# Kernel tuning notes

Hardware: AMD Instinct MI355X
Metric: run time of the kernel (lower is better)

## Reference

```python
import jax, jax.numpy as jnp
import numpy as np

# --- model hyperparams (match init_kwargs) ---
N_DIM = 200      # n_dim == nfeat == nhidden (Linear(200,200) hardcoded in source)
NHID = 200
NLAYERS = 8
ALPHA = 0.1
LAMDA = 0.5
B, L = 20, 100   # dialogues x uniform dialogue length
N = B * L        # 2000 utterances per modality -> 3N = 6000 graph nodes
A_DIM, V_DIM, L_DIM, NSPK = 300, 342, 1024, 2


def _linear_params(key, fin, fout):
    s = 1.0 / np.sqrt(fin)
    k1, k2 = jax.random.split(key)
    W = jax.random.uniform(k1, (fin, fout), jnp.float32, -s, s)
    b = jax.random.uniform(k2, (fout,), jnp.float32, -s, s)
    return W, b


def setup_inputs() -> dict:
    key = jax.random.key(0)
    ks = jax.random.split(key, 12)
    a = jax.random.normal(ks[0], (N, A_DIM), jnp.float32)
    v = jax.random.normal(ks[1], (N, V_DIM), jnp.float32)
    l = jax.random.normal(ks[2], (N, L_DIM), jnp.float32)
    qmask = jax.random.uniform(ks[3], (L, B, NSPK), dtype=jnp.float32)
    # dense normalized adjacency over the 3N-node multimodal graph
    adj = jax.random.uniform(ks[4], (3 * N, 3 * N), dtype=jnp.float32) / (3.0 * N)
    Wa, ba = _linear_params(ks[5], A_DIM, N_DIM)
    Wv, bv = _linear_params(ks[6], V_DIM, N_DIM)
    Wl, bl = _linear_params(ks[7], L_DIM, N_DIM)
    spk_emb = jax.random.normal(ks[8], (NSPK, N_DIM), jnp.float32)
    W0, b0 = _linear_params(ks[9], N_DIM, NHID)
    s = 1.0 / np.sqrt(NHID)
    # variant=True -> conv weight is [2*nhidden, nhidden]
    convW = jax.random.uniform(ks[10], (NLAYERS, 2 * NHID, NHID), jnp.float32, -s, s)
    return dict(a=a, v=v, l=l, qmask=qmask, adj=adj,
                Wa=Wa, ba=ba, Wv=Wv, bv=bv, Wl=Wl, bl=bl,
                spk_emb=spk_emb, W0=W0, b0=b0, convW=convW, dia_len=L)


def reference(a, v, l, qmask, adj, Wa, ba, Wv, bv, Wl, bl, spk_emb, W0, b0, convW, dia_len):
    # modality projections
    a = a @ Wa + ba                                   # [N, n_dim]
    v = v @ Wv + bv
    l = l @ Wl + bl
    # qmask: [L, B, n_spk] seq-first -> concat per dialogue (uniform lengths)
    qcat = jnp.transpose(qmask[:dia_len], (1, 0, 2)).reshape(-1, qmask.shape[-1])  # [N, n_spk]
    spk_idx = jnp.argmax(qcat, axis=-1)
    l = l + spk_emb[spk_idx]                          # use_speaker, 'l' in modals
    # big multimodal graph: stack modalities along node axis
    x = jnp.concatenate([a, v, l], axis=0)            # [3N, n_dim]
    # GCNII_lyc (eval mode: dropout identity)
    h0 = jax.nn.relu(x @ W0 + b0)                     # [3N, nhidden]
    thetas = jnp.log(LAMDA / jnp.arange(1, NLAYERS + 1, dtype=jnp.float32) + 1.0)

    def layer(h, wt):
        W, theta = wt
        hi = adj @ h                                  # spmm (dense here)
        support = jnp.concatenate([hi, h0], axis=1)   # variant=True
        r = (1.0 - ALPHA) * hi + ALPHA * h0
        h_new = jax.nn.relu(theta * (support @ W) + (1.0 - theta) * r)
        return h_new, None

    h, _ = jax.lax.scan(layer, h0, (convW, thetas))
    feat = jnp.concatenate([x, h], axis=1)            # use_residue -> [3N, n_dim+nhidden]
    n = a.shape[0]
    # split modality chunks back and fuse on feature axis -> [N, 3*(n_dim+nhidden)]
    return jnp.concatenate([feat[:n], feat[n:2 * n], feat[2 * n:3 * n]], axis=-1)
```

## Files before the change

kernel.cpp:

```cpp
#include <hip/hip_runtime.h>
#include <math.h>

typedef unsigned short u16;
typedef unsigned int u32;
typedef __bf16 bf8_t __attribute__((ext_vector_type(8)));
typedef float f4_t __attribute__((ext_vector_type(4)));
typedef u16 us8_t __attribute__((ext_vector_type(8)));
typedef u16 us4_t __attribute__((ext_vector_type(4)));

#define LDC 224
#define NROWS 6016
#define PLANE (NROWS*LDC)

__device__ __forceinline__ float b2f(u16 x){
  union{u32 u; float f;} c; c.u = ((u32)x)<<16; return c.f;
}
__device__ __forceinline__ u16 f2b(float f){
  union{u32 u; float f;} c; c.f = f;
  u32 b = c.u;
  return (u16)((b + 0x7FFFu + ((b>>16)&1u)) >> 16);
}
__device__ __forceinline__ u16 ldcvt(const void* p, size_t i, int f){
  return f ? f2b(((const float*)p)[i]) : ((const u16*)p)[i];
}
__device__ __forceinline__ void gl16(const u16* g, u16* l){
  __builtin_amdgcn_global_load_lds((const __attribute__((address_space(1))) void*)g,
                                   (__attribute__((address_space(3))) void*)l, 16, 0, 0);
}

__global__ void detect_kernel(const u16* __restrict__ adj, int* __restrict__ flag)
{
  int l = threadIdx.x;
  u16 u = adj[2*l];
  int ex = (u >> 7) & 0xFF;
  bool ok = ((u >> 15) == 0) && (ex >= 0x30) && (ex <= 0x72);
  unsigned long long m = __ballot(ok);
  if (l == 0) flag[0] = (__popcll(m) < 32) ? 1 : 0;
}

__global__ void conv_kernel(const int* __restrict__ flag, const void* __restrict__ adj,
                            u16* __restrict__ adj_bf)
{
  const int f = flag[0];
  size_t idx = (size_t)blockIdx.x*256 + threadIdx.x;
  if (idx >= (size_t)6016*752) return;
  int row = (int)(idx / 752);
  int k8  = (int)(idx - (size_t)row*752) * 8;
  us8_t vv;
  if (row < 6000){
    if (f){
      const float* src = (const float*)adj + (size_t)row*6000;
      if (k8 + 8 <= 6000){
        f4_t x0 = *(const f4_t*)(src + k8);
        f4_t x1 = *(const f4_t*)(src + k8 + 4);
        #pragma unroll
        for (int j=0;j<4;j++){ vv[j] = f2b(x0[j]); vv[4+j] = f2b(x1[j]); }
      } else {
        #pragma unroll
        for (int j=0;j<8;j++){ int k=k8+j; vv[j] = (k<6000) ? f2b(src[k]) : (u16)0; }
      }
    } else {
      const u16* src = (const u16*)adj + (size_t)row*6000;
      if (k8 + 8 <= 6000){
        vv = *(const us8_t*)(src + k8);
      } else {
        #pragma unroll
        for (int j=0;j<8;j++){ int k=k8+j; vv[j] = (k<6000) ? src[k] : (u16)0; }
      }
    }
  } else {
    #pragma unroll
    for (int j=0;j<8;j++) vv[j] = 0;
  }
  *(us8_t*)(adj_bf + (size_t)row*6016 + k8) = vv;
}

__global__ void prep_kernel(const int* __restrict__ flag,
                            const void* __restrict__ Wa, const void* __restrict__ Wv,
                            const void* __restrict__ Wl, const void* __restrict__ W0,
                            const void* __restrict__ convW, const void* __restrict__ qmask,
                            const void* __restrict__ a_in, const void* __restrict__ v_in,
                            const void* __restrict__ l_in, const void* __restrict__ spkemb_in,
                            const void* __restrict__ ba, const void* __restrict__ bv,
                            const void* __restrict__ bl, const void* __restrict__ b0,
                            u16* __restrict__ WaT, u16* __restrict__ WvT, u16* __restrict__ WlT,
                            u16* __restrict__ W0T, u16* __restrict__ WtT, u16* __restrict__ WbT,
                            int* __restrict__ spk, u16* __restrict__ x_bf,
                            u16* __restrict__ a_p, u16* __restrict__ v_p, u16* __restrict__ l_p,
                            u16* __restrict__ spkem, u16* __restrict__ b_all)
{
  const int f = flag[0];
  const int y = blockIdx.y;
  const int e = blockIdx.x*256 + threadIdx.x;

  if (y < 20){
    const void* src; u16* dst; int K, kpad; size_t soff = 0;
    if (y == 0){ src=Wa; dst=WaT; K=300; kpad=320; }
    else if (y == 1){ src=Wv; dst=WvT; K=342; kpad=384; }
    else if (y == 2){ src=Wl; dst=WlT; K=1024; kpad=1024; }
    else if (y == 3){ src=W0; dst=W0T; K=200; kpad=256; }
    else if (y < 12){ int i=y-4;  src=convW; soff=(size_t)i*80000;          dst=WtT + i*57344; K=200; kpad=256; }
    else            { int i=y-12; src=convW; soff=(size_t)i*80000 + 40000;  dst=WbT + i*57344; K=200; kpad=256; }
    int total = 224*kpad;
    if (e >= total) return;
    int n = e / kpad, k = e - n*kpad;
    u16 val = 0;
    if (k < K && n < 200) val = ldcvt(src, soff + (size_t)k*200 + n, f);
    dst[e] = val;
    return;
  }
  if (y == 20){
    if (e < 2000){
      int b = e/100, t = e - b*100;
      size_t base = ((size_t)t*20 + b)*2;
      bool one;
      if (f) one = ((const float*)qmask)[base+1] > ((const float*)qmask)[base];
      else   one = b2f(((const u16*)qmask)[base+1]) > b2f(((const u16*)qmask)[base]);
      spk[e] = one ? 1 : 0;
    } else if (e < 2400){
      spkem[e-2000] = ldcvt(spkemb_in, e-2000, f);
    } else if (e < 3200){
      int j = e - 2400; int which = j/200, idx = j - which*200;
      const void* src = (which==0)?ba:(which==1)?bv:(which==2)?bl:b0;
      b_all[j] = ldcvt(src, idx, f);
    }
    return;
  }
  if (y == 21){
    if (e < 16*LDC) x_bf[(size_t)6000*LDC + e] = 0;
    return;
  }
  if (y < 25){
    size_t eg = (size_t)(y-22)*229376 + e;
    if (eg >= (size_t)2048*320) return;
    int row = (int)(eg/320), k = (int)(eg - (size_t)row*320);
    a_p[eg] = (row < 2000 && k < 300) ? ldcvt(a_in, (size_t)row*300 + k, f) : (u16)0;
    return;
  }
  if (y < 29){
    size_t eg = (size_t)(y-25)*229376 + e;
    if (eg >= (size_t)2048*384) return;
    int row = (int)(eg/384), k = (int)(eg - (size_t)row*384);
    v_p[eg] = (row < 2000 && k < 342) ? ldcvt(v_in, (size_t)row*342 + k, f) : (u16)0;
    return;
  }
  {
    size_t eg = (size_t)(y-29)*229376 + e;
    if (eg >= (size_t)2048*1024) return;
    int row = (int)(eg >> 10), k = (int)(eg & 1023);
    l_p[eg] = (row < 2000) ? ldcvt(l_in, (size_t)row*1024 + k, f) : (u16)0;
  }
}

template<int WR>
__global__ __launch_bounds__(256, 2)
void gemm_kernel(const int* __restrict__ flag, int dynA,
                 const void* __restrict__ A1, int lda1, int kv1, int kg1, int ks1, const u16* __restrict__ B1, int ldb1,
                 const u16* __restrict__ A2, int lda2, int kv2, int kg2, int ks2, const u16* __restrict__ B2, int ldb2,
                 int Mv, int Mout, int spp, int emode,
                 const u16* __restrict__ bias, const u16* __restrict__ spk_e, const int* __restrict__ spk_idx,
                 u16* __restrict__ part_base,
                 const u16* __restrict__ hi_ro, const u16* __restrict__ h0_ro,
                 float theta,
                 u16* __restrict__ outN, u16* __restrict__ outT)
{
  __shared__ u16 ldsA[WR*32*64];
  __shared__ u16 ldsB[224*64];
  const int fval = dynA ? flag[0] : 0;
  const int tid = threadIdx.x;
  const int l = tid & 63;
  const int w = tid >> 6;
  const int wrow = w >> 1, wcol = w & 1;
  const int row0 = blockIdx.x * (WR*32);
  const int lq = l >> 4, lr = l & 15;

  f4_t acc[WR][7];
  #pragma unroll
  for (int i=0;i<WR;i++)
    #pragma unroll
    for (int j=0;j<7;j++){ f4_t z = {0.f,0.f,0.f,0.f}; acc[i][j] = z; }

  #pragma unroll 1
  for (int pair = 0; pair < 2; ++pair){
    const u16* A16 = pair ? A2 : (const u16*)A1;
    const float* A32 = pair ? nullptr : (const float*)A1;
    const int af32 = pair ? 0 : fval;
    int lda = pair ? lda2 : lda1;
    int kv = pair ? kv2 : kv1;      int ks = pair ? ks2 : ks1;
    int kg = pair ? kg2 : kg1;
    const u16* B = pair ? B2 : B1;  int ldb = pair ? ldb2 : ldb1;
    int sb, se;
    if (pair == 0){ sb = blockIdx.y * spp; se = sb + spp; if (se > ks) se = ks; }
    else { sb = 0; se = ks; }

    #pragma unroll 1
    for (int s = sb; s < se; ++s){
      int k0 = s << 6;
      __syncthreads();
      bool alignedA = ((lda & 7) == 0) && (row0 + WR*32 <= Mv);
      bool gldsA = (!af32) && alignedA && (k0 + 64 <= kg);
      if (gldsA){
        const u16* abase = A16 + k0;
        #pragma unroll
        for (int i=0;i<WR;i++){
          int c = (i<<8) + tid;
          int m = c >> 3, k8p = c & 7;
          int k8 = k8p ^ (m & 7);
          gl16(abase + (size_t)(row0+m)*lda + (k8<<3), &ldsA[c<<3]);
        }
      } else if (af32 && alignedA && (k0 + 64 <= kv)){
        const float* ap = A32 + (size_t)row0*lda + k0;
        #pragma unroll
        for (int i=0;i<WR;i++){
          int c = (i<<8) + tid;
          int m = c >> 3, k8 = c & 7;
          f4_t x0 = *(const f4_t*)(ap + (size_t)m*lda + (k8<<3));
          f4_t x1 = *(const f4_t*)(ap + (size_t)m*lda + (k8<<3) + 4);
          us8_t vv;
          #pragma unroll
          for (int j=0;j<4;j++){ vv[j] = f2b(x0[j]); vv[4+j] = f2b(x1[j]); }
          *(us8_t*)(&ldsA[(m<<6) + ((k8 ^ (m&7))<<3)]) = vv;
        }
      } else {
        #pragma unroll
        for (int i=0;i<WR;i++){
          int c = (i<<8) + tid;
          int m = c >> 3, k8 = c & 7;
          int gr = row0 + m; if (gr > Mv-1) gr = Mv-1;
          us8_t vv;
          #pragma unroll
          for (int j=0;j<8;j++){
            int kk = k0 + (k8<<3) + j;
            u16 t = 0;
            if (kk < kv){
              if (af32) t = f2b(A32[(size_t)gr*lda + kk]);
              else      t = A16[(size_t)gr*lda + kk];
            }
            vv[j] = t;
          }
          *(us8_t*)(&ldsA[(m<<6) + ((k8 ^ (m&7))<<3)]) = vv;
        }
      }
      {
        const u16* bbase = B + k0;
        #pragma unroll
        for (int i=0;i<7;i++){
          int c = (i<<8) + tid;
          int n = c >> 3, k8p = c & 7;
          int k8 = k8p ^ (n & 7);
          gl16(bbase + (size_t)n*ldb + (k8<<3), &ldsB[c<<3]);
        }
      }
      __syncthreads();
      #pragma unroll
      for (int h=0; h<2; ++h){
        bf8_t af[WR], bfr[7];
        int kc = lq + (h<<2);
        #pragma unroll
        for (int rt=0;rt<WR;rt++){
          int m = wrow*(16*WR) + rt*16 + lr;
          af[rt] = *(const bf8_t*)(&ldsA[(m<<6) + ((kc ^ (m&7))<<3)]);
        }
        #pragma unroll
        for (int ct=0;ct<7;ct++){
          int n = wcol*112 + ct*16 + lr;
          bfr[ct] = *(const bf8_t*)(&ldsB[(n<<6) + ((kc ^ (n&7))<<3)]);
        }
        #pragma unroll
        for (int rt=0;rt<WR;rt++)
          #pragma unroll
          for (int ct=0;ct<7;ct++)
            acc[rt][ct] = __builtin_amdgcn_mfma_f32_16x16x32_bf16(af[rt], bfr[ct], acc[rt][ct], 0,0,0);
      }
    }
  }

  #pragma unroll
  for (int rt=0;rt<WR;rt++){
    int r_base = row0 + wrow*(16*WR) + rt*16 + lq*4;
    #pragma unroll
    for (int ct=0;ct<7;ct++){
      int c = wcol*112 + ct*16 + lr;
      f4_t a4 = acc[rt][ct];
      if (emode == 0){
        u16* dst = part_base + (size_t)blockIdx.y * PLANE;
        #pragma unroll
        for (int r=0;r<4;r++) dst[(size_t)(r_base+r)*LDC + c] = f2b(a4[r]);
      } else if (emode == 1){
        float bval = (c < 200) ? b2f(bias[c]) : 0.f;
        #pragma unroll
        for (int r=0;r<4;r++){
          int R = r_base + r;
          if (R < Mout){
            float vv = a4[r] + bval;
            if (spk_e && c < 200) vv += b2f(spk_e[spk_idx[R]*200 + c]);
            outN[(size_t)R*LDC + c] = f2b(vv);
          }
        }
      } else if (emode == 2){
        float bval = (c < 200) ? b2f(bias[c]) : 0.f;
        us4_t p;
        #pragma unroll
        for (int r=0;r<4;r++){
          int R = r_base + r;
          float vv = a4[r] + bval; if (vv < 0.f) vv = 0.f;
          u16 q = f2b(vv);
          outN[(size_t)R*LDC + c] = q;
          p[r] = q;
        }
        *(us4_t*)(&outT[(size_t)c*NROWS + r_base]) = p;
      } else {
        us4_t p;
        #pragma unroll
        for (int r=0;r<4;r++){
          int R = r_base + r;
          size_t ix = (size_t)R*LDC + c;
          float hiv = b2f(hi_ro[ix]), h0v = b2f(h0_ro[ix]);
          float rr = 0.9f*hiv + 0.1f*h0v;
          float vv = theta*a4[r] + (1.f - theta)*rr;
          if (vv < 0.f) vv = 0.f;
          p[r] = f2b(vv);
        }
        *(us4_t*)(&outT[(size_t)c*NROWS + r_base]) = p;
      }
    }
  }
}

__global__ void reduce_kernel(const u16* __restrict__ part, int nsk, u16* __restrict__ hi_bf)
{
  size_t i8 = ((size_t)blockIdx.x*256 + threadIdx.x)*8;
  float s[8];
  #pragma unroll
  for (int j=0;j<8;j++) s[j] = 0.f;
  for (int p=0;p<nsk;p++){
    us8_t v = *(const us8_t*)(part + (size_t)p*PLANE + i8);
    #pragma unroll
    for (int j=0;j<8;j++) s[j] += b2f(v[j]);
  }
  us8_t o;
  #pragma unroll
  for (int j=0;j<8;j++) o[j] = f2b(s[j]);
  *(us8_t*)(hi_bf + i8) = o;
}

__device__ __forceinline__ u16 sent(u16 t, u16 snan, u16 sbig){
  u16 mag = t & 0x7FFF;
  if (mag >= 0x7F80) return snan;
  if (mag >= 0x4480) return sbig;
  return t;
}
__global__ void out_kernel(const int* __restrict__ flag,
                           const u16* __restrict__ x_bf, const u16* __restrict__ hT,
                           void* __restrict__ outp)
{
  __shared__ u16 tile[64*216];
  const int of32 = flag[0];
  u16* o16 = (u16*)outp;
  float* o32 = (float*)outp;
  const int tid = threadIdx.x;
  const int n0 = blockIdx.x*64;
  for (int m=0;m<3;m++){
    for (int cc = tid; cc < 1600; cc += 256){
      int r = cc/25, c8 = cc - r*25;
      int n = n0 + r;
      int rr = n < 2000 ? n : 1999;
      us8_t vv = *(const us8_t*)(x_bf + ((size_t)(m*2000 + rr))*LDC + c8*8);
      #pragma unroll
      for (int j=0;j<8;j++) vv[j] = sent(vv[j], 0x46EA, 0x46DB);
      if (n < 2000){
        size_t off = (size_t)n*1200 + m*400 + c8*8;
        if (!of32) *(us8_t*)(o16 + off) = vv;
        else {
          f4_t lo, hi;
          #pragma unroll
          for (int j=0;j<4;j++){ lo[j] = b2f(vv[j]); hi[j] = b2f(vv[4+j]); }
          *(f4_t*)(o32 + off) = lo; *(f4_t*)(o32 + off + 4) = hi;
        }
      }
    }
    __syncthreads();
    for (int cc = tid; cc < 1600; cc += 256){
      int c = cc >> 3, ng = cc & 7;
      int nb = n0 + ng*8;
      if (nb > 1992) nb = 1992;
      us8_t vv = *(const us8_t*)(hT + (size_t)c*NROWS + m*2000 + nb);
      #pragma unroll
      for (int j=0;j<8;j++) tile[(ng*8+j)*216 + c] = sent(vv[j], 0x469C, 0x468C);
    }
    __syncthreads();
    for (int cc = tid; cc < 1600; cc += 256){
      int r = cc/25, c8 = cc - r*25;
      int n = n0 + r;
      if (n < 2000){
        us8_t vv = *(const us8_t*)(&tile[r*216 + c8*8]);
        size_t off = (size_t)n*1200 + m*400 + 200 + c8*8;
        if (!of32) *(us8_t*)(o16 + off) = vv;
        else {
          f4_t lo, hi;
          #pragma unroll
          for (int j=0;j<4;j++){ lo[j] = b2f(vv[j]); hi[j] = b2f(vv[4+j]); }
          *(f4_t*)(o32 + off) = lo; *(f4_t*)(o32 + off + 4) = hi;
        }
      }
    }
    __syncthreads();
  }
}

extern "C" void kernel_launch(void* const* d_in, const int* in_sizes, int n_in,
                              void* d_out, int out_size, void* d_ws, size_t ws_size,
                              hipStream_t stream)
{
  const void* a     = d_in[0];
  const void* v     = d_in[1];
  const void* l     = d_in[2];
  const void* qmask = d_in[3];
  const void* adj   = d_in[4];
  const void* Wa    = d_in[5];
  const void* ba    = d_in[6];
  const void* Wv    = d_in[7];
  const void* bv    = d_in[8];
  const void* Wl    = d_in[9];
  const void* bl    = d_in[10];
  const void* spk_emb = d_in[11];
  const void* W0    = d_in[12];
  const void* b0    = d_in[13];
  const void* convW = d_in[14];

  int cfg = (ws_size >= (size_t)125*1024*1024) ? 2
          : (ws_size >= (size_t)48*1024*1024) ? 1 : 0;
  const int SK = (cfg >= 1) ? 8 : 2;
  const int SPP = (94 + SK - 1) / SK;

  char* ws = (char*)d_ws;
  size_t off = 0;
  auto alloc = [&](size_t bytes)->char*{
    char* p = ws + off; off = (off + bytes + 255) & ~(size_t)255; return p;
  };
  int*  flag  = (int*) alloc(256);
  u16*  x_bf  = (u16*) alloc((size_t)PLANE*2);
  u16*  h0_bf = (u16*) alloc((size_t)PLANE*2);
  u16*  hi_bf = (u16*) alloc((size_t)PLANE*2);
  u16*  hT    = (u16*) alloc((size_t)PLANE*2);
  u16*  a_p   = (u16*) alloc((size_t)2048*320*2);
  u16*  v_p   = (u16*) alloc((size_t)2048*384*2);
  u16*  l_p   = (u16*) alloc((size_t)2048*1024*2);
  u16* WaT = (u16*)alloc(224*320*2);
  u16* WvT = (u16*)alloc(224*384*2);
  u16* WlT = (u16*)alloc(224*1024*2);
  u16* W0T = (u16*)alloc(224*256*2);
  u16* WtT = (u16*)alloc((size_t)8*224*256*2);
  u16* WbT = (u16*)alloc((size_t)8*224*256*2);
  int* spk = (int*)alloc(2000*4);
  u16* spkem = (u16*)alloc(400*2);
  u16* b_all = (u16*)alloc(800*2);
  u16* part = (u16*)alloc((size_t)SK*PLANE*2);
  u16* adj_bf = (cfg == 2) ? (u16*)alloc((size_t)6016*6016*2) : nullptr;

  detect_kernel<<<1,64,0,stream>>>((const u16*)adj, flag);

  if (cfg == 2)
    conv_kernel<<<dim3(17672),256,0,stream>>>(flag, adj, adj_bf);

  prep_kernel<<<dim3(896,39),256,0,stream>>>(flag, Wa,Wv,Wl,W0,convW,qmask,
      a,v,l,spk_emb, ba,bv,bl,b0,
      WaT,WvT,WlT,W0T,WtT,WbT, spk, x_bf, a_p,v_p,l_p, spkem, b_all);

  gemm_kernel<1><<<dim3(64,1),256,0,stream>>>(flag,0, a_p,320,320,320,5, WaT,320,
      nullptr,0,0,0,0,nullptr,0, 2048,2000, 5, 1, b_all, nullptr, nullptr,
      nullptr, nullptr, nullptr, 0.f, x_bf, nullptr);
  gemm_kernel<1><<<dim3(64,1),256,0,stream>>>(flag,0, v_p,384,384,384,6, WvT,384,
      nullptr,0,0,0,0,nullptr,0, 2048,2000, 6, 1, b_all+200, nullptr, nullptr,
      nullptr, nullptr, nullptr, 0.f, x_bf + (size_t)2000*LDC, nullptr);
  gemm_kernel<1><<<dim3(64,1),256,0,stream>>>(flag,0, l_p,1024,1024,1024,16, WlT,1024,
      nullptr,0,0,0,0,nullptr,0, 2048,2000, 16, 1, b_all+400, spkem, spk,
      nullptr, nullptr, nullptr, 0.f, x_bf + (size_t)4000*LDC, nullptr);

  gemm_kernel<1><<<dim3(188,1),256,0,stream>>>(flag,0, x_bf,LDC,LDC,256,4, W0T,256,
      nullptr,0,0,0,0,nullptr,0, NROWS,NROWS, 4, 2, b_all+600, nullptr, nullptr,
      nullptr, nullptr, nullptr, 0.f, h0_bf, hT);

  for (int i=0;i<8;i++){
    float theta = logf(0.5f/(float)(i+1) + 1.0f);
    if (cfg == 2)
      gemm_kernel<2><<<dim3(94,SK),256,0,stream>>>(flag,0, adj_bf,6016,6016,6016,94, hT,NROWS,
          nullptr,0,0,0,0,nullptr,0, 6016,0, SPP, 0, nullptr, nullptr, nullptr,
          part, nullptr, nullptr, 0.f, nullptr, nullptr);
    else
      gemm_kernel<2><<<dim3(94,SK),256,0,stream>>>(flag,1, adj,6000,6000,0,94, hT,NROWS,
          nullptr,0,0,0,0,nullptr,0, 6000,0, SPP, 0, nullptr, nullptr, nullptr,
          part, nullptr, nullptr, 0.f, nullptr, nullptr);
    reduce_kernel<<<dim3(PLANE/2048),256,0,stream>>>(part, SK, hi_bf);
    gemm_kernel<1><<<dim3(188,1),256,0,stream>>>(flag,0, hi_bf,LDC,LDC,256,4, WtT + (size_t)i*57344,256,
        h0_bf,LDC,LDC,256,4, WbT + (size_t)i*57344,256,
        NROWS,0, 4, 3, nullptr, nullptr, nullptr, nullptr, hi_bf, h0_bf, theta,
        nullptr, hT);
  }

  out_kernel<<<dim3(32),256,0,stream>>>(flag, x_bf, hT, (void*)d_out);
}
```

Measured before the change: 742.2 us.

## Inline dtype detection, fold adj conversion into prep, halve split-K, parallelize output

```diff
diff --git a/kernel.cpp b/kernel.cpp
--- a/kernel.cpp
+++ b/kernel.cpp
@@ -28,54 +28,16 @@
                                    (__attribute__((address_space(3))) void*)l, 16, 0, 0);
 }
 
-__global__ void detect_kernel(const u16* __restrict__ adj, int* __restrict__ flag)
-{
-  int l = threadIdx.x;
+__device__ __forceinline__ int detect_inline(const u16* adj){
+  int l = threadIdx.x & 63;
   u16 u = adj[2*l];
   int ex = (u >> 7) & 0xFF;
   bool ok = ((u >> 15) == 0) && (ex >= 0x30) && (ex <= 0x72);
   unsigned long long m = __ballot(ok);
-  if (l == 0) flag[0] = (__popcll(m) < 32) ? 1 : 0;
-}
-
-__global__ void conv_kernel(const int* __restrict__ flag, const void* __restrict__ adj,
-                            u16* __restrict__ adj_bf)
-{
-  const int f = flag[0];
-  size_t idx = (size_t)blockIdx.x*256 + threadIdx.x;
-  if (idx >= (size_t)6016*752) return;
-  int row = (int)(idx / 752);
-  int k8  = (int)(idx - (size_t)row*752) * 8;
-  us8_t vv;
-  if (row < 6000){
-    if (f){
-      const float* src = (const float*)adj + (size_t)row*6000;
-      if (k8 + 8 <= 6000){
-        f4_t x0 = *(const f4_t*)(src + k8);
-        f4_t x1 = *(const f4_t*)(src + k8 + 4);
-        #pragma unroll
-        for (int j=0;j<4;j++){ vv[j] = f2b(x0[j]); vv[4+j] = f2b(x1[j]); }
-      } else {
-        #pragma unroll
-        for (int j=0;j<8;j++){ int k=k8+j; vv[j] = (k<6000) ? f2b(src[k]) : (u16)0; }
-      }
-    } else {
-      const u16* src = (const u16*)adj + (size_t)row*6000;
-      if (k8 + 8 <= 6000){
-        vv = *(const us8_t*)(src + k8);
-      } else {
-        #pragma unroll
-        for (int j=0;j<8;j++){ int k=k8+j; vv[j] = (k<6000) ? src[k] : (u16)0; }
-      }
-    }
-  } else {
-    #pragma unroll
-    for (int j=0;j<8;j++) vv[j] = 0;
-  }
-  *(us8_t*)(adj_bf + (size_t)row*6016 + k8) = vv;
-}
-
-__global__ void prep_kernel(const int* __restrict__ flag,
+  return (__popcll(m) < 32) ? 1 : 0;
+}
+
+__global__ void prep_kernel(const void* __restrict__ adj, u16* __restrict__ adj_bf,
                             const void* __restrict__ Wa, const void* __restrict__ Wv,
                             const void* __restrict__ Wl, const void* __restrict__ W0,
                             const void* __restrict__ convW, const void* __restrict__ qmask,
@@ -89,9 +51,45 @@
                             u16* __restrict__ a_p, u16* __restrict__ v_p, u16* __restrict__ l_p,
                             u16* __restrict__ spkem, u16* __restrict__ b_all)
 {
-  const int f = flag[0];
+  const int f = detect_inline((const u16*)adj);
   const int y = blockIdx.y;
   const int e = blockIdx.x*256 + threadIdx.x;
+
+  if (y >= 39){
+    if (!adj_bf) return;
+    size_t idx = (size_t)(y-39)*229376 + e;
+    if (idx >= (size_t)6016*752) return;
+    int row = (int)(idx / 752);
+    int k8  = (int)(idx - (size_t)row*752) * 8;
+    us8_t vv;
+    if (row < 6000){
+      if (f){
+        const float* src = (const float*)adj + (size_t)row*6000;
+        if (k8 + 8 <= 6000){
+          f4_t x0 = *(const f4_t*)(src + k8);
+          f4_t x1 = *(const f4_t*)(src + k8 + 4);
+          #pragma unroll
+          for (int j=0;j<4;j++){ vv[j] = f2b(x0[j]); vv[4+j] = f2b(x1[j]); }
+        } else {
+          #pragma unroll
+          for (int j=0;j<8;j++){ int k=k8+j; vv[j] = (k<6000) ? f2b(src[k]) : (u16)0; }
+        }
+      } else {
+        const u16* src = (const u16*)adj + (size_t)row*6000;
+        if (k8 + 8 <= 6000){
+          vv = *(const us8_t*)(src + k8);
+        } else {
+          #pragma unroll
+          for (int j=0;j<8;j++){ int k=k8+j; vv[j] = (k<6000) ? src[k] : (u16)0; }
+        }
+      }
+    } else {
+      #pragma unroll
+      for (int j=0;j<8;j++) vv[j] = 0;
+    }
+    *(us8_t*)(adj_bf + (size_t)row*6016 + k8) = vv;
+    return;
+  }
 
   if (y < 20){
     const void* src; u16* dst; int K, kpad; size_t soff = 0;
@@ -154,7 +152,7 @@
 
 template<int WR>
 __global__ __launch_bounds__(256, 2)
-void gemm_kernel(const int* __restrict__ flag, int dynA,
+void gemm_kernel(int dynA,
                  const void* __restrict__ A1, int lda1, int kv1, int kg1, int ks1, const u16* __restrict__ B1, int ldb1,
                  const u16* __restrict__ A2, int lda2, int kv2, int kg2, int ks2, const u16* __restrict__ B2, int ldb2,
                  int Mv, int Mout, int spp, int emode,
@@ -166,7 +164,7 @@
 {
   __shared__ u16 ldsA[WR*32*64];
   __shared__ u16 ldsB[224*64];
-  const int fval = dynA ? flag[0] : 0;
+  const int fval = dynA ? detect_inline((const u16*)A1) : 0;
   const int tid = threadIdx.x;
   const int l = tid & 63;
   const int w = tid >> 6;
@@ -350,61 +348,58 @@
   if (mag >= 0x4480) return sbig;
   return t;
 }
-__global__ void out_kernel(const int* __restrict__ flag,
+__global__ void out_kernel(const void* __restrict__ adjv,
                            const u16* __restrict__ x_bf, const u16* __restrict__ hT,
                            void* __restrict__ outp)
 {
   __shared__ u16 tile[64*216];
-  const int of32 = flag[0];
+  const int of32 = detect_inline((const u16*)adjv);
   u16* o16 = (u16*)outp;
   float* o32 = (float*)outp;
   const int tid = threadIdx.x;
   const int n0 = blockIdx.x*64;
-  for (int m=0;m<3;m++){
-    for (int cc = tid; cc < 1600; cc += 256){
-      int r = cc/25, c8 = cc - r*25;
-      int n = n0 + r;
-      int rr = n < 2000 ? n : 1999;
-      us8_t vv = *(const us8_t*)(x_bf + ((size_t)(m*2000 + rr))*LDC + c8*8);
-      #pragma unroll
-      for (int j=0;j<8;j++) vv[j] = sent(vv[j], 0x46EA, 0x46DB);
-      if (n < 2000){
-        size_t off = (size_t)n*1200 + m*400 + c8*8;
-        if (!of32) *(us8_t*)(o16 + off) = vv;
-        else {
-          f4_t lo, hi;
-          #pragma unroll
-          for (int j=0;j<4;j++){ lo[j] = b2f(vv[j]); hi[j] = b2f(vv[4+j]); }
-          *(f4_t*)(o32 + off) = lo; *(f4_t*)(o32 + off + 4) = hi;
-        }
-      }
-    }
-    __syncthreads();
-    for (int cc = tid; cc < 1600; cc += 256){
-      int c = cc >> 3, ng = cc & 7;
-      int nb = n0 + ng*8;
-      if (nb > 1992) nb = 1992;
-      us8_t vv = *(const us8_t*)(hT + (size_t)c*NROWS + m*2000 + nb);
-      #pragma unroll
-      for (int j=0;j<8;j++) tile[(ng*8+j)*216 + c] = sent(vv[j], 0x469C, 0x468C);
-    }
-    __syncthreads();
-    for (int cc = tid; cc < 1600; cc += 256){
-      int r = cc/25, c8 = cc - r*25;
-      int n = n0 + r;
-      if (n < 2000){
-        us8_t vv = *(const us8_t*)(&tile[r*216 + c8*8]);
-        size_t off = (size_t)n*1200 + m*400 + 200 + c8*8;
-        if (!of32) *(us8_t*)(o16 + off) = vv;
-        else {
-          f4_t lo, hi;
-          #pragma unroll
-          for (int j=0;j<4;j++){ lo[j] = b2f(vv[j]); hi[j] = b2f(vv[4+j]); }
-          *(f4_t*)(o32 + off) = lo; *(f4_t*)(o32 + off + 4) = hi;
-        }
-      }
-    }
-    __syncthreads();
+  const int m = blockIdx.y;
+  for (int cc = tid; cc < 1600; cc += 256){
+    int r = cc/25, c8 = cc - r*25;
+    int n = n0 + r;
+    int rr = n < 2000 ? n : 1999;
+    us8_t vv = *(const us8_t*)(x_bf + ((size_t)(m*2000 + rr))*LDC + c8*8);
+    #pragma unroll
+    for (int j=0;j<8;j++) vv[j] = sent(vv[j], 0x46EA, 0x46DB);
+    if (n < 2000){
+      size_t off = (size_t)n*1200 + m*400 + c8*8;
+      if (!of32) *(us8_t*)(o16 + off) = vv;
+      else {
+        f4_t lo, hi;
+        #pragma unroll
+        for (int j=0;j<4;j++){ lo[j] = b2f(vv[j]); hi[j] = b2f(vv[4+j]); }
+        *(f4_t*)(o32 + off) = lo; *(f4_t*)(o32 + off + 4) = hi;
+      }
+    }
+  }
+  for (int cc = tid; cc < 1600; cc += 256){
+    int c = cc >> 3, ng = cc & 7;
+    int nb = n0 + ng*8;
+    if (nb > 1992) nb = 1992;
+    us8_t vv = *(const us8_t*)(hT + (size_t)c*NROWS + m*2000 + nb);
+    #pragma unroll
+    for (int j=0;j<8;j++) tile[(ng*8+j)*216 + c] = sent(vv[j], 0x469C, 0x468C);
+  }
+  __syncthreads();
+  for (int cc = tid; cc < 1600; cc += 256){
+    int r = cc/25, c8 = cc - r*25;
+    int n = n0 + r;
+    if (n < 2000){
+      us8_t vv = *(const us8_t*)(&tile[r*216 + c8*8]);
+      size_t off = (size_t)n*1200 + m*400 + 200 + c8*8;
+      if (!of32) *(us8_t*)(o16 + off) = vv;
+      else {
+        f4_t lo, hi;
+        #pragma unroll
+        for (int j=0;j<4;j++){ lo[j] = b2f(vv[j]); hi[j] = b2f(vv[4+j]); }
+        *(f4_t*)(o32 + off) = lo; *(f4_t*)(o32 + off + 4) = hi;
+      }
+    }
   }
 }
 
@@ -430,7 +425,7 @@
 
   int cfg = (ws_size >= (size_t)125*1024*1024) ? 2
           : (ws_size >= (size_t)48*1024*1024) ? 1 : 0;
-  const int SK = (cfg >= 1) ? 8 : 2;
+  const int SK = (cfg >= 1) ? 4 : 2;
   const int SPP = (94 + SK - 1) / SK;
 
   char* ws = (char*)d_ws;
@@ -438,7 +433,6 @@
   auto alloc = [&](size_t bytes)->char*{
     char* p = ws + off; off = (off + bytes + 255) & ~(size_t)255; return p;
   };
-  int*  flag  = (int*) alloc(256);
   u16*  x_bf  = (u16*) alloc((size_t)PLANE*2);
   u16*  h0_bf = (u16*) alloc((size_t)PLANE*2);
   u16*  hi_bf = (u16*) alloc((size_t)PLANE*2);
@@ -458,45 +452,40 @@
   u16* part = (u16*)alloc((size_t)SK*PLANE*2);
   u16* adj_bf = (cfg == 2) ? (u16*)alloc((size_t)6016*6016*2) : nullptr;
 
-  detect_kernel<<<1,64,0,stream>>>((const u16*)adj, flag);
-
-  if (cfg == 2)
-    conv_kernel<<<dim3(17672),256,0,stream>>>(flag, adj, adj_bf);
-
-  prep_kernel<<<dim3(896,39),256,0,stream>>>(flag, Wa,Wv,Wl,W0,convW,qmask,
-      a,v,l,spk_emb, ba,bv,bl,b0,
+  prep_kernel<<<dim3(896, (cfg==2) ? 59 : 39),256,0,stream>>>(adj, adj_bf,
+      Wa,Wv,Wl,W0,convW,qmask, a,v,l,spk_emb, ba,bv,bl,b0,
       WaT,WvT,WlT,W0T,WtT,WbT, spk, x_bf, a_p,v_p,l_p, spkem, b_all);
 
-  gemm_kernel<1><<<dim3(64,1),256,0,stream>>>(flag,0, a_p,320,320,320,5, WaT,320,
+  gemm_kernel<1><<<dim3(64,1),256,0,stream>>>(0, a_p,320,320,320,5, WaT,320,
       nullptr,0,0,0,0,nullptr,0, 2048,2000, 5, 1, b_all, nullptr, nullptr,
       nullptr, nullptr, nullptr, 0.f, x_bf, nullptr);
-  gemm_kernel<1><<<dim3(64,1),256,0,stream>>>(flag,0, v_p,384,384,384,6, WvT,384,
+  gemm_kernel<1><<<dim3(64,1),256,0,stream>>>(0, v_p,384,384,384,6, WvT,384,
       nullptr,0,0,0,0,nullptr,0, 2048,2000, 6, 1, b_all+200, nullptr, nullptr,
       nullptr, nullptr, nullptr, 0.f, x_bf + (size_t)2000*LDC, nullptr);
-  gemm_kernel<1><<<dim3(64,1),256,0,stream>>>(flag,0, l_p,1024,1024,1024,16, WlT,1024,
+  gemm_kernel<1><<<dim3(64,1),256,0,stream>>>(0, l_p,1024,1024,1024,16, WlT,1024,
       nullptr,0,0,0,0,nullptr,0, 2048,2000, 16, 1, b_all+400, spkem, spk,
       nullptr, nullptr, nullptr, 0.f, x_bf + (size_t)4000*LDC, nullptr);
 
-  gemm_kernel<1><<<dim3(188,1),256,0,stream>>>(flag,0, x_bf,LDC,LDC,256,4, W0T,256,
+  gemm_kernel<1><<<dim3(188,1),256,0,stream>>>(0, x_bf,LDC,LDC,256,4, W0T,256,
       nullptr,0,0,0,0,nullptr,0, NROWS,NROWS, 4, 2, b_all+600, nullptr, nullptr,
       nullptr, nullptr, nullptr, 0.f, h0_bf, hT);
 
   for (int i=0;i<8;i++){
     float theta = logf(0.5f/(float)(i+1) + 1.0f);
     if (cfg == 2)
-      gemm_kernel<2><<<dim3(94,SK),256,0,stream>>>(flag,0, adj_bf,6016,6016,6016,94, hT,NROWS,
+      gemm_kernel<2><<<dim3(94,SK),256,0,stream>>>(0, adj_bf,6016,6016,6016,94, hT,NROWS,
           nullptr,0,0,0,0,nullptr,0, 6016,0, SPP, 0, nullptr, nullptr, nullptr,
           part, nullptr, nullptr, 0.f, nullptr, nullptr);
     else
-      gemm_kernel<2><<<dim3(94,SK),256,0,stream>>>(flag,1, adj,6000,6000,0,94, hT,NROWS,
+      gemm_kernel<2><<<dim3(94,SK),256,0,stream>>>(1, adj,6000,6000,0,94, hT,NROWS,
           nullptr,0,0,0,0,nullptr,0, 6000,0, SPP, 0, nullptr, nullptr, nullptr,
           part, nullptr, nullptr, 0.f, nullptr, nullptr);
     reduce_kernel<<<dim3(PLANE/2048),256,0,stream>>>(part, SK, hi_bf);
-    gemm_kernel<1><<<dim3(188,1),256,0,stream>>>(flag,0, hi_bf,LDC,LDC,256,4, WtT + (size_t)i*57344,256,
+    gemm_kernel<1><<<dim3(188,1),256,0,stream>>>(0, hi_bf,LDC,LDC,256,4, WtT + (size_t)i*57344,256,
         h0_bf,LDC,LDC,256,4, WbT + (size_t)i*57344,256,
         NROWS,0, 4, 3, nullptr, nullptr, nullptr, nullptr, hi_bf, h0_bf, theta,
         nullptr, hT);
   }
 
-  out_kernel<<<dim3(32),256,0,stream>>>(flag, x_bf, hT, (void*)d_out);
-}
+  out_kernel<<<dim3(32,3),256,0,stream>>>(adj, x_bf, hT, (void*)d_out);
+}
```

Result: faster. 705.8 us (-4.9%).
